# Optimization experiments

Measured on AMD Instinct MI355X. Metric: run time of the kernel, lower is better.

Reference implementation:

```python
import jax, jax.numpy as jnp
import numpy as np

N_NODES = 100000
N_EDGES = 1600000
DIM = 64

def setup_inputs() -> dict:
    key = jax.random.key(0)
    k1, k2, k3 = jax.random.split(key, 3)
    x = jax.random.normal(k1, (N_NODES, DIM), dtype=jnp.float32)
    edge_index = jax.random.randint(k2, (2, N_EDGES), 0, N_NODES, dtype=jnp.int64)
    edge_weight = jax.random.uniform(k3, (N_EDGES,), dtype=jnp.float32)
    return {"x": x, "edge_index": edge_index, "edge_weight": edge_weight}

def reference(x, edge_index, edge_weight):
    # out[row] += x[col] * edge_weight  (edge-weighted gather + scatter-add)
    row, col = edge_index[0], edge_index[1]
    messages = x[col] * edge_weight[:, None]            # [E, dim]
    out = jax.ops.segment_sum(messages, row, num_segments=x.shape[0])  # [N, dim]
    return out
```

## Files before the change

### kernel.cpp

```cpp
#include <hip/hip_runtime.h>
#include <hip/hip_fp16.h>
#include <stdint.h>


typedef unsigned long long ull;
typedef int   v4i __attribute__((ext_vector_type(4)));
typedef float v4f __attribute__((ext_vector_type(4)));

#define RB      128
#define CAP     2432
#define CHUNK   4096
#define EPT     8
#define SLOTS   48
#define BPAD    16
#define OVF_CAP 65536
#define NBP     1024

__device__ __forceinline__ unsigned short f2bf(float f) {
    union { float f; unsigned int u; } c;
    c.f = f;
    unsigned int lsb = (c.u >> 16) & 1u;
    c.u += 0x7fffu + lsb;
    return (unsigned short)(c.u >> 16);
}
__device__ __forceinline__ float bf2f(unsigned short u) {
    union { unsigned int u; float f; } c;
    c.u = ((unsigned int)u) << 16;
    return c.f;
}
__device__ __forceinline__ unsigned pack_cw(int col, float w) {
    unsigned hb = __half_as_ushort(__float2half(w));
    return (((unsigned)col) << 15) | (hb >> 1);
}
__device__ __forceinline__ float unpack_w(unsigned v) {
    return __half2float(__ushort_as_half((unsigned short)((v & 0x7fffu) << 1)));
}

__global__ __launch_bounds__(512) void prep(
    const int* __restrict__ ei, const float* __restrict__ ew,
    int* __restrict__ bcnt, ull* __restrict__ seg,
    int* __restrict__ ovf_cnt, int3* __restrict__ ovf, int E, int NB,
    int nbin, const float* __restrict__ x, unsigned short* __restrict__ xb,
    int n4)
{
    __shared__ int      hist[NBP];
    __shared__ int      lstart[NBP];
    __shared__ int      gbase[NBP];
    __shared__ int      wsum[8];
    __shared__ ull      sorted[CHUNK];
    __shared__ unsigned gpos[CHUNK];
    int t = threadIdx.x;

    if ((int)blockIdx.x >= nbin) {
        int i0 = ((int)blockIdx.x - nbin) * 4096 + t;
#pragma unroll
        for (int k = 0; k < 8; ++k) {
            int i = i0 + k * 512;
            if (i < n4) {
                v4f v = ((const v4f*)x)[i];
                ushort4 o;
                o.x = f2bf(v.x); o.y = f2bf(v.y);
                o.z = f2bf(v.z); o.w = f2bf(v.w);
                ((ushort4*)xb)[i] = o;
            }
        }
        return;
    }

    for (int i = t; i < NBP; i += 512) hist[i] = 0;
    __syncthreads();

    int e0   = blockIdx.x * CHUNK;
    int nval = E - e0; if (nval > CHUNK) nval = CHUNK;
    bool al4 = ((E & 3) == 0);

    int      rk[EPT];
    unsigned bk[EPT];
    ull      cw[EPT];
    bool     vd[EPT];
#pragma unroll
    for (int j = 0; j < EPT / 4; ++j) {
        int eb = e0 + (j * 512 + t) * 4;
        v4i r4, c4; v4f w4;
        if (al4 && eb + 3 < E) {
            r4 = *(const v4i*)(ei + eb);
            c4 = *(const v4i*)(ei + E + eb);
            w4 = *(const v4f*)(ew + eb);
        } else {
#pragma unroll
            for (int u = 0; u < 4; ++u) {
                int e = eb + u;
                r4[u] = e < E ? ei[e] : 0;
                c4[u] = e < E ? ei[E + e] : 0;
                w4[u] = e < E ? ew[e] : 0.f;
            }
        }
#pragma unroll
        for (int u = 0; u < 4; ++u) {
            int idx = j * 4 + u;
            int e = eb + u;
            vd[idx] = e < E;
            int bkt = r4[u] >> 7;
            int rl  = r4[u] & (RB - 1);
            rk[idx] = vd[idx] ? atomicAdd(&hist[bkt], 1) : 0;
            bk[idx] = (unsigned)bkt;
            cw[idx] = (((ull)__float_as_uint(w4[u])) << 32) |
                      (unsigned)((rl << 17) | c4[u]);
        }
    }
    __syncthreads();

    {
        int a = hist[2 * t], b = hist[2 * t + 1];
        int ps = a + b;
        int lane = t & 63, wid = t >> 6;
        int s = ps;
#pragma unroll
        for (int off = 1; off < 64; off <<= 1) {
            int o = __shfl_up(s, off);
            if (lane >= off) s += o;
        }
        if (lane == 63) wsum[wid] = s;
        __syncthreads();
        if (t < 8) {
            int v = wsum[t];
            int s2 = v;
#pragma unroll
            for (int off = 1; off < 8; off <<= 1) {
                int o = __shfl_up(s2, off);
                if (t >= off) s2 += o;
            }
            wsum[t] = s2 - v;
        }
        __syncthreads();
        int excl = s - ps + wsum[wid];
        lstart[2 * t]     = excl;
        lstart[2 * t + 1] = excl + a;
    }

    for (int i = t; i < NB; i += 512) {
        int h = hist[i];
        gbase[i] = h ? atomicAdd(&bcnt[i * BPAD], h) : 0;
    }
    __syncthreads();

#pragma unroll
    for (int j = 0; j < EPT; ++j) {
        if (!vd[j]) continue;
        int bkt = (int)bk[j];
        int lp  = lstart[bkt] + rk[j];
        sorted[lp] = cw[j];
        int loc = gbase[bkt] + rk[j];
        if (loc < CAP) {
            gpos[lp] = (unsigned)(bkt * CAP + loc);
        } else {
            gpos[lp] = 0xFFFFFFFFu;
            int o = atomicAdd(ovf_cnt, 1);
            if (o < OVF_CAP) {
                unsigned lo = (unsigned)cw[j];
                ovf[o] = make_int3(bkt * RB + ((lo >> 17) & (RB - 1)),
                                   lo & 0x1FFFF, (int)(cw[j] >> 32));
            }
        }
    }
    __syncthreads();

    for (int i = t; i < nval; i += 512) {
        unsigned gp = gpos[i];
        if (gp != 0xFFFFFFFFu) seg[gp] = sorted[i];
    }
}

template <bool BF>
__global__ __launch_bounds__(512, 8) void bucket_acc(
    const void* __restrict__ xv, const ull* __restrict__ seg,
    const int* __restrict__ bcnt, float* __restrict__ out,
    int* __restrict__ ovf_cnt, int3* __restrict__ ovf, int N)
{
    __shared__ int      cur[RB];
    __shared__ unsigned tile[RB * SLOTS];
    int t = threadIdx.x;
    int g = blockIdx.x;
    if (t < RB) cur[t] = 0;
    __syncthreads();

    int c = bcnt[g * BPAD];
    if (c > CAP) c = CAP;
    const ull* base = seg + (size_t)g * CAP;

    for (int i = t; i < c; i += 512) {
        ull e = base[i];
        unsigned lo = (unsigned)e;
        int rl  = (lo >> 17) & (RB - 1);
        int col = lo & 0x1FFFF;
        float w = __int_as_float((int)(e >> 32));
        int pos = atomicAdd(&cur[rl], 1);
        if (pos < SLOTS) {
            tile[rl * SLOTS + pos] = pack_cw(col, w);
        } else {
            int o = atomicAdd(ovf_cnt, 1);
            if (o < OVF_CAP)
                ovf[o] = make_int3(g * RB + rl, col, __float_as_int(w));
        }
    }
    __syncthreads();

    int wid  = t >> 6;
    int lane = t & 63;
    const unsigned short* xh = (const unsigned short*)xv;
    const float*          xf = (const float*)xv;

    for (int k = 0; k < 16; ++k) {
        int r   = wid * 16 + k;
        int row = g * RB + r;
        if (row >= N) break;
        int cc = cur[r];
        if (cc > SLOTS) cc = SLOTS;
        const unsigned* tb = &tile[r * SLOTS];

        float acc = 0.0f;
        int p = 0;
        for (; p + 8 <= cc; p += 8) {
            unsigned a[8]; float xr[8];
#pragma unroll
            for (int i = 0; i < 8; ++i) a[i] = tb[p + i];
#pragma unroll
            for (int i = 0; i < 8; ++i) {
                size_t off = (((size_t)(a[i] >> 15)) << 6) + lane;
                xr[i] = BF ? bf2f(xh[off]) : xf[off];
            }
#pragma unroll
            for (int i = 0; i < 8; ++i)
                acc = fmaf(xr[i], unpack_w(a[i]), acc);
        }
        if (p < cc) {
            unsigned a[8]; float xr[8], w[8];
#pragma unroll
            for (int i = 0; i < 8; ++i) {
                int q = p + i;
                bool valid = q < cc;
                if (!valid) q = cc - 1;
                a[i] = tb[q];
                w[i] = valid ? unpack_w(a[i]) : 0.0f;
            }
#pragma unroll
            for (int i = 0; i < 8; ++i) {
                size_t off = (((size_t)(a[i] >> 15)) << 6) + lane;
                xr[i] = BF ? bf2f(xh[off]) : xf[off];
            }
#pragma unroll
            for (int i = 0; i < 8; ++i) acc = fmaf(xr[i], w[i], acc);
        }
        __builtin_nontemporal_store(acc, out + (((size_t)row) << 6) + lane);
    }
}

template <bool BF>
__global__ __launch_bounds__(256) void ovf_apply(
    const void* __restrict__ xv, const int* __restrict__ ovf_cnt,
    const int3* __restrict__ ovf, float* __restrict__ out)
{
    int n = *ovf_cnt;
    if (n > OVF_CAP) n = OVF_CAP;
    int wid  = (blockIdx.x * 256 + threadIdx.x) >> 6;
    int lane = threadIdx.x & 63;
    int nw   = gridDim.x * 4;
    for (int o = wid; o < n; o += nw) {
        int3 tt = ovf[o];
        float w = __int_as_float(tt.z);
        size_t off = (((size_t)tt.y) << 6) + lane;
        float x = BF ? bf2f(((const unsigned short*)xv)[off])
                     : ((const float*)xv)[off];
        atomicAdd(&out[(((size_t)tt.x) << 6) + lane], x * w);
    }
}

__global__ __launch_bounds__(256) void scatter_edges(
    const float* __restrict__ x, const int* __restrict__ ei,
    const float* __restrict__ ew, float* __restrict__ out, int E)
{
    long long idx = (long long)blockIdx.x * 256 + threadIdx.x;
    int e = (int)(idx >> 4);
    if (e >= E) return;
    int j = (int)(idx & 15);
    int row = ei[e];
    int col = ei[E + e];
    float w = ew[e];
    v4f v = *(const v4f*)(x + (((size_t)col) << 6) + (j << 2));
    float* op = out + (((size_t)row) << 6) + (j << 2);
    atomicAdd(op + 0, v.x * w);
    atomicAdd(op + 1, v.y * w);
    atomicAdd(op + 2, v.z * w);
    atomicAdd(op + 3, v.w * w);
}

extern "C" void kernel_launch(void* const* d_in, const int* in_sizes, int n_in,
                              void* d_out, int out_size, void* d_ws, size_t ws_size,
                              hipStream_t stream) {
    const float* x  = (const float*)d_in[0];
    const int*   ei = (const int*)d_in[1];
    const float* ew = (const float*)d_in[2];
    float*       out = (float*)d_out;

    int E = in_sizes[2];
    int N = out_size / 64;
    int NB = (N + RB - 1) / RB;

    size_t ovf_base  = (size_t)NB * BPAD + 2;
    size_t xb_base   = (ovf_base + 3 * (size_t)OVF_CAP + 3) & ~(size_t)3;
    size_t xb_ints   = (size_t)N * 32;
    size_t seg_ints  = (size_t)NB * CAP * 2;

    size_t seg_base_bf = (xb_base + xb_ints + 1) & ~(size_t)1;
    size_t need_bf     = (seg_base_bf + seg_ints) * 4;

    size_t seg_base_f  = (xb_base + 1) & ~(size_t)1;
    size_t need_f      = (seg_base_f + seg_ints) * 4;

    int nbin  = (E + CHUNK - 1) / CHUNK;
    int n4    = (N * 64) / 4;
    int nconv = (n4 + 4095) / 4096;

    if ((ws_size >= need_bf || ws_size >= need_f) && N <= (1 << 17)) {
        bool use_bf = ws_size >= need_bf;
        int* w32 = (int*)d_ws;
        int* bcnt = w32;
        int* ovf_cnt = w32 + NB * BPAD;
        int3* ovf = (int3*)(w32 + ovf_base);
        unsigned short* xb = (unsigned short*)(w32 + xb_base);
        ull* seg = (ull*)(w32 + (use_bf ? seg_base_bf : seg_base_f));

        (void)hipMemsetAsync(w32, 0, ((size_t)NB * BPAD + 2) * sizeof(int),
                             stream);

        if (use_bf) {
            prep<<<nbin + nconv, 512, 0, stream>>>(
                ei, ew, bcnt, seg, ovf_cnt, ovf, E, NB, nbin, x, xb, n4);
            bucket_acc<true><<<NB, 512, 0, stream>>>(
                xb, seg, bcnt, out, ovf_cnt, ovf, N);
            ovf_apply<true><<<64, 256, 0, stream>>>(xb, ovf_cnt, ovf, out);
        } else {
            prep<<<nbin, 512, 0, stream>>>(
                ei, ew, bcnt, seg, ovf_cnt, ovf, E, NB, nbin, x, xb, 0);
            bucket_acc<false><<<NB, 512, 0, stream>>>(
                x, seg, bcnt, out, ovf_cnt, ovf, N);
            ovf_apply<false><<<64, 256, 0, stream>>>(x, ovf_cnt, ovf, out);
        }
    } else {
        (void)hipMemsetAsync(out, 0, (size_t)out_size * sizeof(float), stream);
        long long threads = (long long)E * 16;
        scatter_edges<<<(int)((threads + 255) / 256), 256, 0, stream>>>(
            x, ei, ew, out, E);
    }
}
```

Baseline: 168.3 us.

## Halve row bucket size and compact intermediate edge records to five bytes

```diff
diff --git a/kernel.cpp b/kernel.cpp
--- a/kernel.cpp
+++ b/kernel.cpp
@@ -6,15 +6,16 @@
 typedef unsigned long long ull;
 typedef int   v4i __attribute__((ext_vector_type(4)));
 typedef float v4f __attribute__((ext_vector_type(4)));
-
-#define RB      128
-#define CAP     2432
+typedef unsigned char uchar;
+
+#define RB      64
+#define CAP     1280
 #define CHUNK   4096
 #define EPT     8
 #define SLOTS   48
 #define BPAD    16
 #define OVF_CAP 65536
-#define NBP     1024
+#define NBP     2048
 
 __device__ __forceinline__ unsigned short f2bf(float f) {
     union { float f; unsigned int u; } c;
@@ -38,7 +39,8 @@
 
 __global__ __launch_bounds__(512) void prep(
     const int* __restrict__ ei, const float* __restrict__ ew,
-    int* __restrict__ bcnt, ull* __restrict__ seg,
+    int* __restrict__ bcnt, unsigned* __restrict__ s4g,
+    uchar* __restrict__ srg,
     int* __restrict__ ovf_cnt, int3* __restrict__ ovf, int E, int NB,
     int nbin, const float* __restrict__ x, unsigned short* __restrict__ xb,
     int n4)
@@ -47,7 +49,8 @@
     __shared__ int      lstart[NBP];
     __shared__ int      gbase[NBP];
     __shared__ int      wsum[8];
-    __shared__ ull      sorted[CHUNK];
+    __shared__ unsigned s4_l[CHUNK];
+    __shared__ uchar    sr_l[CHUNK];
     __shared__ unsigned gpos[CHUNK];
     int t = threadIdx.x;
 
@@ -75,8 +78,8 @@
     bool al4 = ((E & 3) == 0);
 
     int      rk[EPT];
-    unsigned bk[EPT];
-    ull      cw[EPT];
+    unsigned br[EPT];
+    unsigned p4[EPT];
     bool     vd[EPT];
 #pragma unroll
     for (int j = 0; j < EPT / 4; ++j) {
@@ -100,19 +103,18 @@
             int idx = j * 4 + u;
             int e = eb + u;
             vd[idx] = e < E;
-            int bkt = r4[u] >> 7;
-            int rl  = r4[u] & (RB - 1);
+            int bkt = r4[u] >> 6;
             rk[idx] = vd[idx] ? atomicAdd(&hist[bkt], 1) : 0;
-            bk[idx] = (unsigned)bkt;
-            cw[idx] = (((ull)__float_as_uint(w4[u])) << 32) |
-                      (unsigned)((rl << 17) | c4[u]);
+            br[idx] = (unsigned)((bkt << 6) | (r4[u] & (RB - 1)));
+            p4[idx] = pack_cw(c4[u], w4[u]);
         }
     }
     __syncthreads();
 
     {
-        int a = hist[2 * t], b = hist[2 * t + 1];
-        int ps = a + b;
+        int h0 = hist[4 * t],     h1 = hist[4 * t + 1];
+        int h2 = hist[4 * t + 2], h3 = hist[4 * t + 3];
+        int ps = h0 + h1 + h2 + h3;
         int lane = t & 63, wid = t >> 6;
         int s = ps;
 #pragma unroll
@@ -134,8 +136,10 @@
         }
         __syncthreads();
         int excl = s - ps + wsum[wid];
-        lstart[2 * t]     = excl;
-        lstart[2 * t + 1] = excl + a;
+        lstart[4 * t]     = excl;
+        lstart[4 * t + 1] = excl + h0;
+        lstart[4 * t + 2] = excl + h0 + h1;
+        lstart[4 * t + 3] = excl + h0 + h1 + h2;
     }
 
     for (int i = t; i < NB; i += 512) {
@@ -147,33 +151,37 @@
 #pragma unroll
     for (int j = 0; j < EPT; ++j) {
         if (!vd[j]) continue;
-        int bkt = (int)bk[j];
+        int bkt = (int)(br[j] >> 6);
         int lp  = lstart[bkt] + rk[j];
-        sorted[lp] = cw[j];
+        s4_l[lp] = p4[j];
+        sr_l[lp] = (uchar)(br[j] & (RB - 1));
         int loc = gbase[bkt] + rk[j];
         if (loc < CAP) {
             gpos[lp] = (unsigned)(bkt * CAP + loc);
         } else {
             gpos[lp] = 0xFFFFFFFFu;
             int o = atomicAdd(ovf_cnt, 1);
-            if (o < OVF_CAP) {
-                unsigned lo = (unsigned)cw[j];
-                ovf[o] = make_int3(bkt * RB + ((lo >> 17) & (RB - 1)),
-                                   lo & 0x1FFFF, (int)(cw[j] >> 32));
-            }
+            if (o < OVF_CAP)
+                ovf[o] = make_int3(bkt * RB + (int)(br[j] & (RB - 1)),
+                                   (int)(p4[j] >> 15),
+                                   __float_as_int(unpack_w(p4[j])));
         }
     }
     __syncthreads();
 
     for (int i = t; i < nval; i += 512) {
         unsigned gp = gpos[i];
-        if (gp != 0xFFFFFFFFu) seg[gp] = sorted[i];
+        if (gp != 0xFFFFFFFFu) {
+            s4g[gp] = s4_l[i];
+            srg[gp] = sr_l[i];
+        }
     }
 }
 
 template <bool BF>
-__global__ __launch_bounds__(512, 8) void bucket_acc(
-    const void* __restrict__ xv, const ull* __restrict__ seg,
+__global__ __launch_bounds__(256, 8) void bucket_acc(
+    const void* __restrict__ xv, const unsigned* __restrict__ s4g,
+    const uchar* __restrict__ srg,
     const int* __restrict__ bcnt, float* __restrict__ out,
     int* __restrict__ ovf_cnt, int3* __restrict__ ovf, int N)
 {
@@ -186,21 +194,20 @@
 
     int c = bcnt[g * BPAD];
     if (c > CAP) c = CAP;
-    const ull* base = seg + (size_t)g * CAP;
-
-    for (int i = t; i < c; i += 512) {
-        ull e = base[i];
-        unsigned lo = (unsigned)e;
-        int rl  = (lo >> 17) & (RB - 1);
-        int col = lo & 0x1FFFF;
-        float w = __int_as_float((int)(e >> 32));
+    const unsigned* b4 = s4g + (size_t)g * CAP;
+    const uchar*    br = srg + (size_t)g * CAP;
+
+    for (int i = t; i < c; i += 256) {
+        unsigned p4 = b4[i];
+        int rl = br[i];
         int pos = atomicAdd(&cur[rl], 1);
         if (pos < SLOTS) {
-            tile[rl * SLOTS + pos] = pack_cw(col, w);
+            tile[rl * SLOTS + pos] = p4;
         } else {
             int o = atomicAdd(ovf_cnt, 1);
             if (o < OVF_CAP)
-                ovf[o] = make_int3(g * RB + rl, col, __float_as_int(w));
+                ovf[o] = make_int3(g * RB + rl, (int)(p4 >> 15),
+                                   __float_as_int(unpack_w(p4)));
         }
     }
     __syncthreads();
@@ -309,13 +316,16 @@
     size_t ovf_base  = (size_t)NB * BPAD + 2;
     size_t xb_base   = (ovf_base + 3 * (size_t)OVF_CAP + 3) & ~(size_t)3;
     size_t xb_ints   = (size_t)N * 32;
-    size_t seg_ints  = (size_t)NB * CAP * 2;
-
-    size_t seg_base_bf = (xb_base + xb_ints + 1) & ~(size_t)1;
-    size_t need_bf     = (seg_base_bf + seg_ints) * 4;
-
-    size_t seg_base_f  = (xb_base + 1) & ~(size_t)1;
-    size_t need_f      = (seg_base_f + seg_ints) * 4;
+    size_t s4_ints   = (size_t)NB * CAP;
+    size_t sr_ints   = ((size_t)NB * CAP + 3) / 4;
+
+    size_t s4_base_bf  = xb_base + xb_ints;
+    size_t sr_base_bf  = s4_base_bf + s4_ints;
+    size_t need_bf     = (sr_base_bf + sr_ints) * 4;
+
+    size_t s4_base_f   = xb_base;
+    size_t sr_base_f   = s4_base_f + s4_ints;
+    size_t need_f      = (sr_base_f + sr_ints) * 4;
 
     int nbin  = (E + CHUNK - 1) / CHUNK;
     int n4    = (N * 64) / 4;
@@ -328,22 +338,23 @@
         int* ovf_cnt = w32 + NB * BPAD;
         int3* ovf = (int3*)(w32 + ovf_base);
         unsigned short* xb = (unsigned short*)(w32 + xb_base);
-        ull* seg = (ull*)(w32 + (use_bf ? seg_base_bf : seg_base_f));
+        unsigned* s4g = (unsigned*)(w32 + (use_bf ? s4_base_bf : s4_base_f));
+        uchar*    srg = (uchar*)(w32 + (use_bf ? sr_base_bf : sr_base_f));
 
         (void)hipMemsetAsync(w32, 0, ((size_t)NB * BPAD + 2) * sizeof(int),
                              stream);
 
         if (use_bf) {
             prep<<<nbin + nconv, 512, 0, stream>>>(
-                ei, ew, bcnt, seg, ovf_cnt, ovf, E, NB, nbin, x, xb, n4);
-            bucket_acc<true><<<NB, 512, 0, stream>>>(
-                xb, seg, bcnt, out, ovf_cnt, ovf, N);
+                ei, ew, bcnt, s4g, srg, ovf_cnt, ovf, E, NB, nbin, x, xb, n4);
+            bucket_acc<true><<<NB, 256, 0, stream>>>(
+                xb, s4g, srg, bcnt, out, ovf_cnt, ovf, N);
             ovf_apply<true><<<64, 256, 0, stream>>>(xb, ovf_cnt, ovf, out);
         } else {
             prep<<<nbin, 512, 0, stream>>>(
-                ei, ew, bcnt, seg, ovf_cnt, ovf, E, NB, nbin, x, xb, 0);
-            bucket_acc<false><<<NB, 512, 0, stream>>>(
-                x, seg, bcnt, out, ovf_cnt, ovf, N);
+                ei, ew, bcnt, s4g, srg, ovf_cnt, ovf, E, NB, nbin, x, xb, 0);
+            bucket_acc<false><<<NB, 256, 0, stream>>>(
+                x, s4g, srg, bcnt, out, ovf_cnt, ovf, N);
             ovf_apply<false><<<64, 256, 0, stream>>>(x, ovf_cnt, ovf, out);
         }
     } else {
```

Result: slower. 181.4 us (+7.8%).
